# Performance work log

Measured on AMD Instinct MI355X. Metric: run time of the kernel, lower is better.

The kernel has to match this reference:

```python
import jax, jax.numpy as jnp
import numpy as np

N, S, SKV, K, V = 16, 4096, 4096, 64, 64


def setup_inputs() -> dict:
    key = jax.random.key(0)
    k1, k2, k3, k4 = jax.random.split(key, 4)
    return {
        "queries": jax.random.normal(k1, (N, S, K), dtype=jnp.float32),
        "keys": jax.random.normal(k2, (N, SKV, K), dtype=jnp.float32),
        "values": jax.random.normal(k3, (N, SKV, V), dtype=jnp.float32),
        "mask": jax.random.normal(k4, (S, SKV), dtype=jnp.float32),
    }


def reference(queries, keys, values, mask):
    # queries scaled by K^{-1/2}, then baddbmm(mask, q, k^T)
    scale = queries.shape[-1] ** -0.5
    q = queries * scale
    # scores: [N, S, SKV]; mask (S, SKV) broadcasts over batch like baddbmm
    scores = jnp.einsum('nsk,ntk->nst', q, keys) + mask
    attn_weights = jax.nn.softmax(scores, axis=-1)
    # attn: [N, S, V]; dropout_p = 0.0 (eval), needs_weights = False
    attn = jnp.einsum('nst,ntv->nsv', attn_weights, values)
    return attn
```

## Files before the change

### kernel.cpp

```cpp
#include <hip/hip_runtime.h>
#include <cstdint>
#include <cstddef>


typedef __attribute__((ext_vector_type(8))) short short8;
typedef __attribute__((ext_vector_type(4))) short short4v;
typedef __attribute__((ext_vector_type(4))) float f32x4;
typedef __attribute__((ext_vector_type(4))) unsigned int uint4v;
typedef __attribute__((ext_vector_type(2))) unsigned int uint2v;

#define DEV __device__ __forceinline__

constexpr int N_B   = 16;
constexpr int S_Q   = 4096;
constexpr int S_KV  = 4096;
constexpr int DH    = 64;
constexpr int BQ    = 128;
constexpr int BK    = 64;
constexpr int ITERS = S_KV / BK;
constexpr int KSTR  = 72;
constexpr int VSTR  = 68;

#define LOG2E 1.44269504088896340736f

DEV unsigned short f2bf(float f) {
  union { float f; unsigned int i; } x; x.f = f;
  unsigned int r = x.i + 0x7FFFu + ((x.i >> 16) & 1u);
  return (unsigned short)(r >> 16);
}

#if __has_builtin(__builtin_amdgcn_cvt_pk_bf16_f32)
typedef __attribute__((ext_vector_type(2))) __bf16 bf16x2v;
DEV unsigned int packrne(float a, float b) {
  union { bf16x2v v; unsigned int u; } x;
  x.v = __builtin_amdgcn_cvt_pk_bf16_f32(a, b);
  return x.u;
}
#else
DEV unsigned int packrne(float a, float b) {
  union { float f; unsigned int u; } ua, ub; ua.f = a; ub.f = b;
  unsigned int ra = ua.u + 0x7FFFu + ((ua.u >> 16) & 1u);
  unsigned int rb = ub.u + 0x7FFFu + ((ub.u >> 16) & 1u);
  return __builtin_amdgcn_perm(rb, ra, 0x07060302u);
}
#endif

DEV f32x4 mfma16(short4v a, short4v b, f32x4 c) {
#if __has_builtin(__builtin_amdgcn_mfma_f32_16x16x16bf16_1k)
  return __builtin_amdgcn_mfma_f32_16x16x16bf16_1k(a, b, c, 0, 0, 0);
#elif __has_builtin(__builtin_amdgcn_mfma_f32_16x16x16_bf16)
  return __builtin_amdgcn_mfma_f32_16x16x16_bf16(a, b, c, 0, 0, 0);
#else
  asm volatile("v_mfma_f32_16x16x16_bf16 %0, %1, %2, %0\n\ts_nop 7\n\ts_nop 7"
               : "+v"(c) : "v"(a), "v"(b));
  return c;
#endif
}

DEV void stageK(unsigned short* buf, const f32x4* kA, int t) {
  const int r0 = t >> 3, c = t & 7;
  uint4v d0, d1;
  d0[0] = packrne(kA[0][0], kA[0][1]); d0[1] = packrne(kA[0][2], kA[0][3]);
  d0[2] = packrne(kA[1][0], kA[1][1]); d0[3] = packrne(kA[1][2], kA[1][3]);
  d1[0] = packrne(kA[2][0], kA[2][1]); d1[1] = packrne(kA[2][2], kA[2][3]);
  d1[2] = packrne(kA[3][0], kA[3][1]); d1[3] = packrne(kA[3][2], kA[3][3]);
  *(uint4v*)&buf[r0 * KSTR + c * 8]        = d0;
  *(uint4v*)&buf[(r0 + 32) * KSTR + c * 8] = d1;
}

DEV void stageV(unsigned short* buf, const f32x4* L, int t) {
  const int a = t >> 4;
  const int x = t & 15;
  const int slot = (a + x) & 15;
#pragma unroll
  for (int j = 0; j < 4; ++j) {
    uint2v d;
    d[0] = packrne(L[0][j], L[1][j]);
    d[1] = packrne(L[2][j], L[3][j]);
    *(uint2v*)&buf[(x * 4 + j) * VSTR + slot * 4] = d;
  }
}

__global__ __launch_bounds__(256, 2)
void sdpa_fwd(const float* __restrict__ Qg,
              const float* __restrict__ Kg,
              const float* __restrict__ Vg,
              const float* __restrict__ Mg,
              float* __restrict__ Og)
{
  __shared__ __align__(16) unsigned short ldsK[2][BK * KSTR];
  __shared__ __align__(16) unsigned short ldsV[2][DH * VSTR];

  const int n    = blockIdx.y;
  const int q0   = blockIdx.x * BQ;
  const int t    = threadIdx.x;
  const int w    = t >> 6;
  const int lane = t & 63;
  const int l15  = lane & 15;
  const int quad = lane >> 4;

  short8 qfA0, qfA1, qfB0, qfB1;
  {
    const float* qp =
        Qg + ((size_t)n * S_Q + (size_t)(q0 + w * 32 + l15)) * DH + quad * 8;
#pragma unroll
    for (int j = 0; j < 8; ++j) {
      qfA0[j] = (short)f2bf(qp[j]);
      qfA1[j] = (short)f2bf(qp[32 + j]);
      qfB0[j] = (short)f2bf(qp[16 * DH + j]);
      qfB1[j] = (short)f2bf(qp[16 * DH + 32 + j]);
    }
  }

  const float* kgp = Kg + ((size_t)n * S_KV + (t >> 3)) * DH + (t & 7) * 8;
  const float* vgp =
      Vg + ((size_t)n * S_KV + (size_t)(t >> 4) * 4) * DH + (t & 15) * 4;
  const float* mrowA = Mg + (size_t)(q0 + w * 32 + l15) * S_KV + quad * 4;
  const float* mrowB = mrowA + (size_t)16 * S_KV;

  f32x4 accA[4], accB[4];
#pragma unroll
  for (int nt = 0; nt < 4; ++nt)
#pragma unroll
    for (int r = 0; r < 4; ++r) { accA[nt][r] = 0.0f; accB[nt][r] = 0.0f; }
  float lrunA = 0.0f, lrunB = 0.0f;

  f32x4 kA[4], vL[4];
  kA[0] = *(const f32x4*)(kgp);
  kA[1] = *(const f32x4*)(kgp + 4);
  kA[2] = *(const f32x4*)(kgp + 32 * DH);
  kA[3] = *(const f32x4*)(kgp + 32 * DH + 4);
#pragma unroll
  for (int i = 0; i < 4; ++i) vL[i] = *(const f32x4*)(vgp + i * DH);
  stageK(&ldsK[0][0], kA, t);
  stageV(&ldsV[0][0], vL, t);
  __syncthreads();

  for (int it = 0; it < ITERS; ++it) {
    const int p   = it & 1;
    const int kv0 = it * BK;
    const bool more = (it + 1 < ITERS);

    if (more) {
      const float* kn = kgp + (size_t)(kv0 + BK) * DH;
      kA[0] = *(const f32x4*)(kn);
      kA[1] = *(const f32x4*)(kn + 4);
      kA[2] = *(const f32x4*)(kn + 32 * DH);
      kA[3] = *(const f32x4*)(kn + 32 * DH + 4);
      const float* vn = vgp + (size_t)(kv0 + BK) * DH;
#pragma unroll
      for (int i = 0; i < 4; ++i) vL[i] = *(const f32x4*)(vn + i * DH);
    }

    f32x4 mkA[4], mkB[4];
#pragma unroll
    for (int h = 0; h < 4; ++h) {
      mkA[h] = *(const f32x4*)(mrowA + kv0 + 16 * h);
      mkB[h] = *(const f32x4*)(mrowB + kv0 + 16 * h);
    }

    short8 kf[4][2];
#pragma unroll
    for (int h = 0; h < 4; ++h)
#pragma unroll
      for (int kk = 0; kk < 2; ++kk)
        kf[h][kk] =
            *(const short8*)&ldsK[p][(l15 + 16 * h) * KSTR + (quad + 4 * kk) * 8];

    float pvA[4][4], pvB[4][4];
    float rsA = 0.0f, rsB = 0.0f;
#pragma unroll
    for (int h = 0; h < 4; ++h) {
      f32x4 cA = {0.f, 0.f, 0.f, 0.f}, cB = {0.f, 0.f, 0.f, 0.f};
      cA = __builtin_amdgcn_mfma_f32_16x16x32_bf16(kf[h][0], qfA0, cA, 0, 0, 0);
      cB = __builtin_amdgcn_mfma_f32_16x16x32_bf16(kf[h][0], qfB0, cB, 0, 0, 0);
      cA = __builtin_amdgcn_mfma_f32_16x16x32_bf16(kf[h][1], qfA1, cA, 0, 0, 0);
      cB = __builtin_amdgcn_mfma_f32_16x16x32_bf16(kf[h][1], qfB1, cB, 0, 0, 0);
#pragma unroll
      for (int r = 0; r < 4; ++r) {
        float eA = __builtin_amdgcn_exp2f(fmaf(cA[r], 0.125f, mkA[h][r]) * LOG2E);
        float eB = __builtin_amdgcn_exp2f(fmaf(cB[r], 0.125f, mkB[h][r]) * LOG2E);
        pvA[h][r] = eA; rsA += eA;
        pvB[h][r] = eB; rsB += eB;
      }
    }
    rsA += __shfl_xor(rsA, 16, 64);
    rsA += __shfl_xor(rsA, 32, 64);
    rsB += __shfl_xor(rsB, 16, 64);
    rsB += __shfl_xor(rsB, 32, 64);
    lrunA += rsA;
    lrunB += rsB;

    short4v pfA[4], pfB[4];
#pragma unroll
    for (int h = 0; h < 4; ++h) {
      union { uint2v u; short4v s; } ua, ub;
      ua.u[0] = packrne(pvA[h][0], pvA[h][1]);
      ua.u[1] = packrne(pvA[h][2], pvA[h][3]);
      ub.u[0] = packrne(pvB[h][0], pvB[h][1]);
      ub.u[1] = packrne(pvB[h][2], pvB[h][3]);
      pfA[h] = ua.s; pfB[h] = ub.s;
    }

#pragma unroll
    for (int nt = 0; nt < 4; ++nt) {
      const int vcol = l15 + 16 * nt;
      const int xr   = (l15 >> 2) + 4 * nt;
#pragma unroll
      for (int h = 0; h < 4; ++h) {
        const int slot = ((4 * h + quad) + xr) & 15;
        short4v vf = *(const short4v*)&ldsV[p][vcol * VSTR + slot * 4];
        accA[nt] = mfma16(vf, pfA[h], accA[nt]);
        accB[nt] = mfma16(vf, pfB[h], accB[nt]);
      }
    }

    if (more) {
      stageK(&ldsK[p ^ 1][0], kA, t);
      stageV(&ldsV[p ^ 1][0], vL, t);
    }
    __syncthreads();
  }

  const float invA = 1.0f / lrunA;
  const float invB = 1.0f / lrunB;
  float* obA = Og + ((size_t)n * S_Q + (size_t)(q0 + w * 32 + l15)) * DH
             + quad * 4;
  float* obB = obA + (size_t)16 * DH;
#pragma unroll
  for (int nt = 0; nt < 4; ++nt) {
    f32x4 oA, oB;
#pragma unroll
    for (int r = 0; r < 4; ++r) {
      oA[r] = accA[nt][r] * invA;
      oB[r] = accB[nt][r] * invB;
    }
    *(f32x4*)(obA + 16 * nt) = oA;
    *(f32x4*)(obB + 16 * nt) = oB;
  }
}

extern "C" void kernel_launch(void* const* d_in, const int* in_sizes, int n_in,
                              void* d_out, int out_size, void* d_ws, size_t ws_size,
                              hipStream_t stream) {
  (void)in_sizes; (void)n_in; (void)d_ws; (void)ws_size; (void)out_size;
  const float* q = (const float*)d_in[0];
  const float* k = (const float*)d_in[1];
  const float* v = (const float*)d_in[2];
  const float* m = (const float*)d_in[3];
  float* o = (float*)d_out;

  dim3 grid(S_Q / BQ, N_B);
  dim3 block(256);
  hipLaunchKernelGGL(sdpa_fwd, grid, block, 0, stream, q, k, v, m, o);
}
```

Baseline: 308.9 us.

## Split KV range across two blocks and combine partial outputs

Splits the KV sequence into two halves handled by separate blocks (grid z=2). Each block writes unnormalized partial outputs and row sums to the workspace, and a second kernel sums and normalizes them. The aim is more parallelism: 1024 blocks instead of 512 on the many-CU device, with the launch-bounds occupancy hint raised to 4. The cost is an extra kernel launch and extra global traffic for about 32MB of partials. There is no running-max subtraction, and the code keeps relying on that for both halves.

Result: slower. 466.8 us (+51.1%).

```diff
diff --git a/kernel.cpp b/kernel.cpp
--- a/kernel.cpp
+++ b/kernel.cpp
@@ -17,9 +17,13 @@
 constexpr int DH    = 64;
 constexpr int BQ    = 128;
 constexpr int BK    = 64;
-constexpr int ITERS = S_KV / BK;
 constexpr int KSTR  = 72;
 constexpr int VSTR  = 68;
+constexpr int QBLK  = S_Q / BQ;
+
+constexpr size_t OPART_ELEMS = 2ull * N_B * QBLK * BQ * DH;
+constexpr size_t LPART_ELEMS = 2ull * N_B * QBLK * BQ;
+constexpr size_t WS_NEED = (OPART_ELEMS + LPART_ELEMS) * 4;
 
 #define LOG2E 1.44269504088896340736f
 
@@ -81,18 +85,24 @@
   }
 }
 
-__global__ __launch_bounds__(256, 2)
+template <bool SPLIT>
+__global__ __launch_bounds__(256, 4)
 void sdpa_fwd(const float* __restrict__ Qg,
               const float* __restrict__ Kg,
               const float* __restrict__ Vg,
               const float* __restrict__ Mg,
-              float* __restrict__ Og)
+              float* __restrict__ Og,
+              float* __restrict__ Opart,
+              float* __restrict__ Lpart)
 {
   __shared__ __align__(16) unsigned short ldsK[2][BK * KSTR];
   __shared__ __align__(16) unsigned short ldsV[2][DH * VSTR];
 
   const int n    = blockIdx.y;
   const int q0   = blockIdx.x * BQ;
+  const int z    = SPLIT ? blockIdx.z : 0;
+  const int kvb  = z * (S_KV / 2);
+  const int ITERS = SPLIT ? (S_KV / 2 / BK) : (S_KV / BK);
   const int t    = threadIdx.x;
   const int w    = t >> 6;
   const int lane = t & 63;
@@ -112,10 +122,12 @@
     }
   }
 
-  const float* kgp = Kg + ((size_t)n * S_KV + (t >> 3)) * DH + (t & 7) * 8;
+  const float* kgp =
+      Kg + ((size_t)n * S_KV + kvb + (t >> 3)) * DH + (t & 7) * 8;
   const float* vgp =
-      Vg + ((size_t)n * S_KV + (size_t)(t >> 4) * 4) * DH + (t & 15) * 4;
-  const float* mrowA = Mg + (size_t)(q0 + w * 32 + l15) * S_KV + quad * 4;
+      Vg + ((size_t)n * S_KV + kvb + (size_t)(t >> 4) * 4) * DH + (t & 15) * 4;
+  const float* mrowA =
+      Mg + (size_t)(q0 + w * 32 + l15) * S_KV + kvb + quad * 4;
   const float* mrowB = mrowA + (size_t)16 * S_KV;
 
   f32x4 accA[4], accB[4];
@@ -222,35 +234,87 @@
     __syncthreads();
   }
 
-  const float invA = 1.0f / lrunA;
-  const float invB = 1.0f / lrunB;
-  float* obA = Og + ((size_t)n * S_Q + (size_t)(q0 + w * 32 + l15)) * DH
-             + quad * 4;
-  float* obB = obA + (size_t)16 * DH;
-#pragma unroll
-  for (int nt = 0; nt < 4; ++nt) {
-    f32x4 oA, oB;
-#pragma unroll
-    for (int r = 0; r < 4; ++r) {
-      oA[r] = accA[nt][r] * invA;
-      oB[r] = accB[nt][r] * invB;
-    }
-    *(f32x4*)(obA + 16 * nt) = oA;
-    *(f32x4*)(obB + 16 * nt) = oB;
-  }
+  if constexpr (SPLIT) {
+    const int pb = (z * N_B + n) * QBLK + blockIdx.x;
+    float* obA = Opart + (((size_t)pb * BQ) + w * 32 + l15) * DH + quad * 4;
+    float* obB = obA + (size_t)16 * DH;
+#pragma unroll
+    for (int nt = 0; nt < 4; ++nt) {
+      f32x4 oA, oB;
+#pragma unroll
+      for (int r = 0; r < 4; ++r) { oA[r] = accA[nt][r]; oB[r] = accB[nt][r]; }
+      *(f32x4*)(obA + 16 * nt) = oA;
+      *(f32x4*)(obB + 16 * nt) = oB;
+    }
+    if (quad == 0) {
+      Lpart[(size_t)pb * BQ + w * 32 + l15]      = lrunA;
+      Lpart[(size_t)pb * BQ + w * 32 + l15 + 16] = lrunB;
+    }
+  } else {
+    const float invA = 1.0f / lrunA;
+    const float invB = 1.0f / lrunB;
+    float* obA = Og + ((size_t)n * S_Q + (size_t)(q0 + w * 32 + l15)) * DH
+               + quad * 4;
+    float* obB = obA + (size_t)16 * DH;
+#pragma unroll
+    for (int nt = 0; nt < 4; ++nt) {
+      f32x4 oA, oB;
+#pragma unroll
+      for (int r = 0; r < 4; ++r) {
+        oA[r] = accA[nt][r] * invA;
+        oB[r] = accB[nt][r] * invB;
+      }
+      *(f32x4*)(obA + 16 * nt) = oA;
+      *(f32x4*)(obB + 16 * nt) = oB;
+    }
+  }
+}
+
+__global__ __launch_bounds__(256)
+void sdpa_combine(const float* __restrict__ Op, const float* __restrict__ Lp,
+                  float* __restrict__ Og)
+{
+  const int t2 = blockIdx.x * 256 + threadIdx.x;
+  const int vg = t2 & 15;
+  const int qg = (t2 >> 4) & (S_Q - 1);
+  const int n  = t2 >> 16;
+  const int bx = qg >> 7, ql = qg & (BQ - 1);
+  const size_t half = (size_t)N_B * QBLK * BQ * DH;
+  const size_t base = ((((size_t)n * QBLK) + bx) * BQ + ql) * DH + vg * 4;
+  f32x4 a = *(const f32x4*)(Op + base);
+  f32x4 b = *(const f32x4*)(Op + half + base);
+  const size_t lhalf = (size_t)N_B * QBLK * BQ;
+  float l = Lp[((size_t)n * QBLK + bx) * BQ + ql]
+          + Lp[lhalf + ((size_t)n * QBLK + bx) * BQ + ql];
+  const float inv = 1.0f / l;
+  f32x4 o;
+#pragma unroll
+  for (int r = 0; r < 4; ++r) o[r] = (a[r] + b[r]) * inv;
+  *(f32x4*)(Og + (size_t)t2 * 4) = o;
 }
 
 extern "C" void kernel_launch(void* const* d_in, const int* in_sizes, int n_in,
                               void* d_out, int out_size, void* d_ws, size_t ws_size,
                               hipStream_t stream) {
-  (void)in_sizes; (void)n_in; (void)d_ws; (void)ws_size; (void)out_size;
+  (void)in_sizes; (void)n_in; (void)out_size;
   const float* q = (const float*)d_in[0];
   const float* k = (const float*)d_in[1];
   const float* v = (const float*)d_in[2];
   const float* m = (const float*)d_in[3];
   float* o = (float*)d_out;
 
-  dim3 grid(S_Q / BQ, N_B);
-  dim3 block(256);
-  hipLaunchKernelGGL(sdpa_fwd, grid, block, 0, stream, q, k, v, m, o);
-}
+  if (ws_size >= WS_NEED) {
+    float* opart = (float*)d_ws;
+    float* lpart = opart + OPART_ELEMS;
+    dim3 grid(QBLK, N_B, 2);
+    hipLaunchKernelGGL((sdpa_fwd<true>), grid, dim3(256), 0, stream,
+                       q, k, v, m, o, opart, lpart);
+    const int total4 = N_B * S_Q * DH / 4;
+    hipLaunchKernelGGL(sdpa_combine, dim3(total4 / 256), dim3(256), 0, stream,
+                       opart, lpart, o);
+  } else {
+    dim3 grid(QBLK, N_B, 1);
+    hipLaunchKernelGGL((sdpa_fwd<false>), grid, dim3(256), 0, stream,
+                       q, k, v, m, o, nullptr, nullptr);
+  }
+}
```
